# Kernel optimization log

Hardware: AMD Instinct MI355X
Metric: run time of the kernel (lower is better)

Reference implementation:

```python
import jax, jax.numpy as jnp
import numpy as np

N = 102400      # total nodes
B = 1024        # graphs in batch
NPG = 100       # nodes per graph
EPG = 1600      # edges per graph (avg degree 16)
E = B * EPG
D = 512
L = 3
EPS = 1e-5
SLOPE = 0.1     # LeakyReLU negative slope


def setup_inputs() -> dict:
    key = jax.random.key(0)
    k = jax.random.split(key, 6)
    node_feats = jax.random.normal(k[0], (N, D), dtype=jnp.float32)
    # within-graph random edges
    base = jnp.repeat(jnp.arange(B, dtype=jnp.int32) * NPG, EPG)  # [E]
    src = base + jax.random.randint(k[1], (E,), 0, NPG)
    dst = base + jax.random.randint(k[2], (E,), 0, NPG)
    graph_ids = jnp.repeat(jnp.arange(B, dtype=jnp.int32), NPG)   # [N]
    W = jax.random.normal(k[3], (L, D, D), dtype=jnp.float32) * 0.02
    gamma = jnp.ones((L, D), dtype=jnp.float32)
    beta = jnp.zeros((L, D), dtype=jnp.float32)
    lambdas = jnp.ones((L, 3), dtype=jnp.float32)
    return {"node_feats": node_feats, "src": src, "dst": dst,
            "graph_ids": graph_ids, "W": W, "gamma": gamma,
            "beta": beta, "lambdas": lambdas}


def _leaky(x):
    return jnp.where(x > 0, x, SLOPE * x)


def _united_norm(x, graph_ids, gamma, beta, lam):
    # combination of batch / graph / node standardizations, weighted by
    # learnable lambdas, then a shared affine (UnitedNormCommon).
    # batch norm over all nodes (training statistics, biased var)
    mu_b = x.mean(0)
    var_b = x.var(0)
    bn = (x - mu_b) * jax.lax.rsqrt(var_b + EPS)
    # graph norm: stats per graph segment
    mu_g = jax.ops.segment_sum(x, graph_ids, num_segments=B) / NPG
    ex2 = jax.ops.segment_sum(x * x, graph_ids, num_segments=B) / NPG
    var_g = ex2 - mu_g * mu_g
    gn = (x - mu_g[graph_ids]) * jax.lax.rsqrt(var_g + EPS)[graph_ids]
    # node norm: stats per node over feature dim
    mu_n = x.mean(-1, keepdims=True)
    var_n = x.var(-1, keepdims=True)
    nn_ = (x - mu_n) * jax.lax.rsqrt(var_n + EPS)
    mix = lam[0] * bn + lam[1] * gn + lam[2] * nn_
    return gamma * mix + beta


def reference(node_feats, src, dst, graph_ids, W, gamma, beta, lambdas):
    ones_e = jnp.ones((E,), dtype=node_feats.dtype)
    deg_out = jnp.clip(jax.ops.segment_sum(ones_e, src, num_segments=N), 1.0)
    deg_in = jnp.clip(jax.ops.segment_sum(ones_e, dst, num_segments=N), 1.0)
    c_out = jax.lax.rsqrt(deg_out)[:, None]  # D_out^{-1/2}
    c_in = jax.lax.rsqrt(deg_in)[:, None]    # D_in^{-1/2}

    h = node_feats
    embeddings = []
    for l in range(L):
        # GraphConv norm='both', bias=False: D_in^{-1/2} A D_out^{-1/2} h W
        msg = jax.ops.segment_sum((h * c_out)[src], dst, num_segments=N)
        h = (msg * c_in) @ W[l]
        h = _united_norm(h, graph_ids, gamma[l], beta[l], lambdas[l])
        h = _leaky(h)            # dropout=0 -> identity
        # dgl.mean_nodes readout per graph
        embeddings.append(jax.ops.segment_sum(h, graph_ids, num_segments=B) / NPG)
    out = jnp.concatenate(embeddings, axis=-1)   # JumpingKnowledge 'cat' -> [B, 3*D]
    return _leaky(out)
```

## Files before the change

### kernel.cpp

```cpp
#include <hip/hip_runtime.h>
#include <math.h>

#define NN 102400
#define BG 1024
#define NPG 100
#define EPG 1600
#define EE (BG*EPG)
#define DD 512
#define EPSN 1e-5f
#define SLOPE 0.1f

typedef short bf16x8 __attribute__((ext_vector_type(8)));
typedef float f32x4 __attribute__((ext_vector_type(4)));
typedef __attribute__((address_space(1))) const unsigned int gu32;
typedef __attribute__((address_space(3))) unsigned int lu32;

__device__ __forceinline__ void split_bf16(float v, unsigned short& hi, unsigned short& lo) {
    unsigned u = __float_as_uint(v);
    unsigned r = (u + 0x7FFFu + ((u >> 16) & 1u)) >> 16;
    hi = (unsigned short)r;
    float l = v - __uint_as_float(r << 16);
    unsigned ul = __float_as_uint(l);
    unsigned rl = (ul + 0x7FFFu + ((ul >> 16) & 1u)) >> 16;
    lo = (unsigned short)rl;
}


__global__ __launch_bounds__(256) void k_degrees(const int* __restrict__ src,
                                                 const int* __restrict__ dst,
                                                 float* degOut, float* degIn) {
    int e = blockIdx.x * 256 + threadIdx.x;
    atomicAdd(&degOut[src[e]], 1.0f);
    atomicAdd(&degIn[dst[e]], 1.0f);
}

__global__ __launch_bounds__(256) void k_deg_to_c(float* cOut, float* cIn) {
    int i = blockIdx.x * 256 + threadIdx.x;
    float a = cOut[i]; a = a < 1.0f ? 1.0f : a;
    cOut[i] = 1.0f / sqrtf(a);
    float b = cIn[i]; b = b < 1.0f ? 1.0f : b;
    cIn[i] = 1.0f / sqrtf(b);
}

__global__ __launch_bounds__(256) void k_build_A(const int* __restrict__ src,
                                                 const int* __restrict__ dst,
                                                 float* __restrict__ A) {
    int e = blockIdx.x * 256 + threadIdx.x;
    int s = src[e], d = dst[e];
    int g = s / NPG;
    int u = s - g * NPG;
    int v = d - g * NPG;
    atomicAdd(&A[(size_t)g * (NPG*NPG) + v * NPG + u], 1.0f);
}

__global__ __launch_bounds__(256) void k_scale_A(float* __restrict__ A,
                                                 const float* __restrict__ cOut,
                                                 const float* __restrict__ cIn) {
    int idx = blockIdx.x * 256 + threadIdx.x;
    int g = idx / (NPG*NPG);
    int r = idx - g * (NPG*NPG);
    int v = r / NPG;
    int u = r - v * NPG;
    A[idx] *= cIn[g*NPG + v] * cOut[g*NPG + u];
}

__global__ __launch_bounds__(256) void k_prepW(const float* __restrict__ W,
        unsigned short* __restrict__ wHiT, unsigned short* __restrict__ wLoT) {
    __shared__ float tile[64][65];
    int b = blockIdx.x;
    int l = b >> 6;
    int r8 = b & 63;
    int ko = (r8 >> 3) * 64, no = (r8 & 7) * 64;
    const float* Wl = W + (size_t)l * DD * DD;
    int t = threadIdx.x;
    #pragma unroll
    for (int i = 0; i < 16; ++i) {
        int idx = i * 256 + t;
        int r = idx >> 6, c = idx & 63;
        tile[r][c] = Wl[(size_t)(ko + r) * DD + no + c];
    }
    __syncthreads();
    size_t obase = (size_t)l * DD * DD;
    #pragma unroll
    for (int i = 0; i < 16; ++i) {
        int idx = i * 256 + t;
        int r = idx >> 6, c = idx & 63;
        float v = tile[c][r];
        unsigned short hi, lo;
        split_bf16(v, hi, lo);
        wHiT[obase + (size_t)(no + r) * DD + ko + c] = hi;
        wLoT[obase + (size_t)(no + r) * DD + ko + c] = lo;
    }
}


#define GG_DC 32

__global__ __launch_bounds__(256) void k_graph_gemm(const float* __restrict__ A,
                                                    const float* __restrict__ h,
                                                    unsigned short* __restrict__ msgHi,
                                                    unsigned short* __restrict__ msgLo) {
    __shared__ float As[NPG][108];
    __shared__ float hs[NPG][GG_DC];
    int g = blockIdx.x, tid = threadIdx.x;
    const float* Ag = A + (size_t)g * (NPG*NPG);
    size_t hbase = (size_t)g * NPG * DD;

    for (int i = tid; i < NPG*NPG; i += 256) {
        int v = i / NPG;
        As[v][i - v*NPG] = Ag[i];
    }

    int tx = tid & 7;
    int ty = tid >> 3;
    int v0 = ty * 4;

    for (int d0 = 0; d0 < DD; d0 += GG_DC) {
        int i0 = tid, i1 = tid + 256, i2 = tid + 512, i3 = tid + 768;
        float4 t0, t1, t2, t3;
        t0 = *(const float4*)&h[hbase + (size_t)(i0 >> 3) * DD + d0 + (i0 & 7) * 4];
        t1 = *(const float4*)&h[hbase + (size_t)(i1 >> 3) * DD + d0 + (i1 & 7) * 4];
        t2 = *(const float4*)&h[hbase + (size_t)(i2 >> 3) * DD + d0 + (i2 & 7) * 4];
        if (tid < 32)
            t3 = *(const float4*)&h[hbase + (size_t)(i3 >> 3) * DD + d0 + (i3 & 7) * 4];
        __syncthreads();
        *(float4*)&hs[i0 >> 3][(i0 & 7) * 4] = t0;
        *(float4*)&hs[i1 >> 3][(i1 & 7) * 4] = t1;
        *(float4*)&hs[i2 >> 3][(i2 & 7) * 4] = t2;
        if (tid < 32) *(float4*)&hs[i3 >> 3][(i3 & 7) * 4] = t3;
        __syncthreads();

        if (v0 < NPG) {
            float4 acc0 = make_float4(0,0,0,0);
            float4 acc1 = acc0, acc2 = acc0, acc3 = acc0;
            for (int u0 = 0; u0 < NPG; u0 += 4) {
                float4 a0 = *(float4*)&As[v0+0][u0];
                float4 a1 = *(float4*)&As[v0+1][u0];
                float4 a2 = *(float4*)&As[v0+2][u0];
                float4 a3 = *(float4*)&As[v0+3][u0];
                float4 h0 = *(float4*)&hs[u0+0][tx*4];
                float4 h1 = *(float4*)&hs[u0+1][tx*4];
                float4 h2 = *(float4*)&hs[u0+2][tx*4];
                float4 h3 = *(float4*)&hs[u0+3][tx*4];
#define GACC(ACC, AV) \
    ACC.x = fmaf(AV.x, h0.x, fmaf(AV.y, h1.x, fmaf(AV.z, h2.x, fmaf(AV.w, h3.x, ACC.x)))); \
    ACC.y = fmaf(AV.x, h0.y, fmaf(AV.y, h1.y, fmaf(AV.z, h2.y, fmaf(AV.w, h3.y, ACC.y)))); \
    ACC.z = fmaf(AV.x, h0.z, fmaf(AV.y, h1.z, fmaf(AV.z, h2.z, fmaf(AV.w, h3.z, ACC.z)))); \
    ACC.w = fmaf(AV.x, h0.w, fmaf(AV.y, h1.w, fmaf(AV.z, h2.w, fmaf(AV.w, h3.w, ACC.w))));
                GACC(acc0, a0) GACC(acc1, a1) GACC(acc2, a2) GACC(acc3, a3)
#undef GACC
            }
#define STORE_HL(ACC, ROW) { \
            ushort4 h4, l4; \
            split_bf16(ACC.x, h4.x, l4.x); split_bf16(ACC.y, h4.y, l4.y); \
            split_bf16(ACC.z, h4.z, l4.z); split_bf16(ACC.w, h4.w, l4.w); \
            *(ushort4*)&msgHi[hbase + (size_t)(ROW)*DD + d0 + tx*4] = h4; \
            *(ushort4*)&msgLo[hbase + (size_t)(ROW)*DD + d0 + tx*4] = l4; }
            STORE_HL(acc0, v0+0) STORE_HL(acc1, v0+1)
            STORE_HL(acc2, v0+2) STORE_HL(acc3, v0+3)
#undef STORE_HL
        }
    }
}


__global__ __launch_bounds__(256) void k_mfma_gemm(
        const unsigned short* __restrict__ aHi, const unsigned short* __restrict__ aLo,
        const unsigned short* __restrict__ bHiT, const unsigned short* __restrict__ bLoT,
        float* __restrict__ C) {
    __shared__ unsigned short lds[8192];
    int bx = blockIdx.x;
    int m0 = (bx >> 2) << 7;
    int n0 = (bx & 3) << 7;
    int tid = threadIdx.x;
    int wid = tid >> 6, lane = tid & 63;
    int wr = wid >> 1, wc = wid & 1;
    int lr = lane & 15, lk = (lane >> 4) * 8;

    f32x4 zero = {0.f, 0.f, 0.f, 0.f};
    f32x4 acc[4][4];
    #pragma unroll
    for (int i = 0; i < 4; ++i)
        #pragma unroll
        for (int j = 0; j < 4; ++j) acc[i][j] = zero;

    int rA0 = tid >> 2,           kq0 = (tid & 3) * 8;
    int rA1 = (tid + 256) >> 2,   kq1 = (tid & 3) * 8;
    unsigned short* lA0 = lds + wid * 512;
    unsigned short* lA1 = lds + 2048 + wid * 512;
    unsigned short* lB0 = lds + 4096 + wid * 512;
    unsigned short* lB1 = lds + 6144 + wid * 512;

    for (int kt = 0; kt < 48; ++kt) {
        int part = kt >> 4;
        const unsigned short* pA = (part == 1) ? aLo : aHi;
        const unsigned short* pB = (part == 2) ? bLoT : bHiT;
        int kl = (kt & 15) << 5;
        __syncthreads();
        __builtin_amdgcn_global_load_lds((gu32*)(pA + (size_t)(m0 + rA0) * DD + kl + kq0),
                                         (lu32*)lA0, 16, 0, 0);
        __builtin_amdgcn_global_load_lds((gu32*)(pA + (size_t)(m0 + rA1) * DD + kl + kq1),
                                         (lu32*)lA1, 16, 0, 0);
        __builtin_amdgcn_global_load_lds((gu32*)(pB + (size_t)(n0 + rA0) * DD + kl + kq0),
                                         (lu32*)lB0, 16, 0, 0);
        __builtin_amdgcn_global_load_lds((gu32*)(pB + (size_t)(n0 + rA1) * DD + kl + kq1),
                                         (lu32*)lB1, 16, 0, 0);
        __syncthreads();

        bf16x8 af[4], bfr[4];
        #pragma unroll
        for (int i = 0; i < 4; ++i) {
            af[i]  = *(const bf16x8*)(lds + (wr*64 + i*16 + lr) * 32 + lk);
            bfr[i] = *(const bf16x8*)(lds + 4096 + (wc*64 + i*16 + lr) * 32 + lk);
        }
        #pragma unroll
        for (int mi = 0; mi < 4; ++mi)
            #pragma unroll
            for (int ni = 0; ni < 4; ++ni)
                acc[mi][ni] = __builtin_amdgcn_mfma_f32_16x16x32_bf16(
                                  af[mi], bfr[ni], acc[mi][ni], 0, 0, 0);
    }

    #pragma unroll
    for (int mi = 0; mi < 4; ++mi) {
        int row0 = wr*64 + mi*16 + (lane >> 4) * 4;
        #pragma unroll
        for (int j = 0; j < 4; ++j) {
            int row = m0 + row0 + j;
            int col = n0 + wc*64 + lr;
            #pragma unroll
            for (int ni = 0; ni < 4; ++ni)
                C[(size_t)row * DD + col + ni*16] = acc[mi][ni][j];
        }
    }
}


__global__ __launch_bounds__(256) void k_stats(const float* __restrict__ x,
        float* __restrict__ mug, float* __restrict__ rsg,
        float* __restrict__ sumb, float* __restrict__ sumq) {
    int g = blockIdx.x, tid = threadIdx.x;
    size_t base = (size_t)g * NPG * DD;
    float s0 = 0, q0 = 0, s1 = 0, q1 = 0;
    for (int v = 0; v < NPG; ++v) {
        float a = x[base + (size_t)v*DD + tid];
        float b = x[base + (size_t)v*DD + tid + 256];
        s0 += a; q0 = fmaf(a, a, q0);
        s1 += b; q1 = fmaf(b, b, q1);
    }
    const float inv = 1.0f / NPG;
    float m0 = s0 * inv, m1 = s1 * inv;
    mug[(size_t)g*DD + tid]       = m0;
    mug[(size_t)g*DD + tid + 256] = m1;
    rsg[(size_t)g*DD + tid]       = 1.0f / sqrtf(fmaf(-m0, m0, q0*inv) + EPSN);
    rsg[(size_t)g*DD + tid + 256] = 1.0f / sqrtf(fmaf(-m1, m1, q1*inv) + EPSN);
    atomicAdd(&sumb[tid],       s0);
    atomicAdd(&sumq[tid],       q0);
    atomicAdd(&sumb[tid + 256], s1);
    atomicAdd(&sumq[tid + 256], q1);
}


__global__ __launch_bounds__(256) void k_norm(float* __restrict__ x,
        const float* __restrict__ mug, const float* __restrict__ rsg,
        const float* __restrict__ sumb, const float* __restrict__ sumq,
        const float* __restrict__ gamma, const float* __restrict__ beta,
        const float* __restrict__ lam, float* __restrict__ out, int l) {
    __shared__ float emb[4][DD];
    int g = blockIdx.x, tid = threadIdx.x;
    int lane = tid & 63, wave = tid >> 6;
    int cb = lane * 8;
    float l0 = lam[0], l1 = lam[1], l2 = lam[2];
    const float invN = 1.0f / NN;

    float P[8], Q[8], R[8];
    #pragma unroll
    for (int j = 0; j < 8; ++j) {
        int c = cb + j;
        float gm = gamma[c], bt = beta[c];
        float mg = mug[(size_t)g*DD + c], rg = rsg[(size_t)g*DD + c];
        float mb = sumb[c] * invN;
        float rb = 1.0f / sqrtf(fmaf(-mb, mb, sumq[c]*invN) + EPSN);
        P[j] = gm * (l0*rb + l1*rg);
        Q[j] = bt - gm * (l0*mb*rb + l1*mg*rg);
        R[j] = gm * l2;
    }

    float av[8];
    #pragma unroll
    for (int j = 0; j < 8; ++j) av[j] = 0.f;

    size_t base = (size_t)g * NPG * DD;
    for (int v = wave; v < NPG; v += 4) {
        float* rp = x + base + (size_t)v*DD + cb;
        float4 r0 = *(float4*)rp;
        float4 r1 = *(float4*)(rp + 4);
        float vals[8] = {r0.x, r0.y, r0.z, r0.w, r1.x, r1.y, r1.z, r1.w};
        float s = 0, q = 0;
        #pragma unroll
        for (int j = 0; j < 8; ++j) { s += vals[j]; q = fmaf(vals[j], vals[j], q); }
        #pragma unroll
        for (int off = 1; off < 64; off <<= 1) {
            s += __shfl_xor(s, off, 64);
            q += __shfl_xor(q, off, 64);
        }
        float mn = s * (1.0f/DD);
        float rn = 1.0f / sqrtf(fmaf(-mn, mn, q*(1.0f/DD)) + EPSN);
        float o[8];
        #pragma unroll
        for (int j = 0; j < 8; ++j) {
            float xv = vals[j];
            float nn = (xv - mn) * rn;
            float y = fmaf(P[j], xv, fmaf(R[j], nn, Q[j]));
            y = y > 0.f ? y : SLOPE * y;
            o[j] = y;
            av[j] += y;
        }
        *(float4*)rp       = make_float4(o[0], o[1], o[2], o[3]);
        *(float4*)(rp + 4) = make_float4(o[4], o[5], o[6], o[7]);
    }
    #pragma unroll
    for (int j = 0; j < 8; ++j) emb[wave][cb + j] = av[j];
    __syncthreads();
    for (int c = tid; c < DD; c += 256) {
        float e = (emb[0][c] + emb[1][c] + emb[2][c] + emb[3][c]) * (1.0f/NPG);
        e = e > 0.f ? e : SLOPE * e;
        out[(size_t)g * (3*DD) + l*DD + c] = e;
    }
}


extern "C" void kernel_launch(void* const* d_in, const int* in_sizes, int n_in,
                              void* d_out, int out_size, void* d_ws, size_t ws_size,
                              hipStream_t stream) {
    const float* nodeF   = (const float*)d_in[0];
    const int*   src     = (const int*)d_in[1];
    const int*   dst     = (const int*)d_in[2];
    const float* W       = (const float*)d_in[4];
    const float* gamma   = (const float*)d_in[5];
    const float* beta    = (const float*)d_in[6];
    const float* lambdas = (const float*)d_in[7];
    float* out = (float*)d_out;

    float* ws   = (float*)d_ws;
    float* cOut = ws;
    float* cIn  = cOut + NN;
    float* Abuf = cIn + NN;
    float* bufH = Abuf + (size_t)BG*NPG*NPG;
    float* mug  = bufH + (size_t)NN*DD;
    float* rsg  = mug  + (size_t)BG*DD;
    float* sumb = rsg  + (size_t)BG*DD;
    float* sumq = sumb + DD;
    unsigned short* msgHi = (unsigned short*)(sumq + DD);
    unsigned short* msgLo = msgHi + (size_t)NN*DD;
    unsigned short* wHiT  = msgLo + (size_t)NN*DD;
    unsigned short* wLoT  = wHiT  + (size_t)3*DD*DD;

    hipMemsetAsync(cOut, 0, 2*(size_t)NN*sizeof(float), stream);
    hipMemsetAsync(Abuf, 0, (size_t)BG*NPG*NPG*sizeof(float), stream);
    k_degrees<<<EE/256, 256, 0, stream>>>(src, dst, cOut, cIn);
    k_deg_to_c<<<NN/256, 256, 0, stream>>>(cOut, cIn);
    k_build_A<<<EE/256, 256, 0, stream>>>(src, dst, Abuf);
    k_scale_A<<<(BG*NPG*NPG)/256, 256, 0, stream>>>(Abuf, cOut, cIn);
    k_prepW<<<192, 256, 0, stream>>>(W, wHiT, wLoT);

    const float* hcur = nodeF;
    for (int l = 0; l < 3; ++l) {
        k_graph_gemm<<<BG, 256, 0, stream>>>(Abuf, hcur, msgHi, msgLo);
        k_mfma_gemm<<<(NN/128)*(DD/128), 256, 0, stream>>>(
            msgHi, msgLo, wHiT + (size_t)l*DD*DD, wLoT + (size_t)l*DD*DD, bufH);
        hipMemsetAsync(sumb, 0, 2*DD*sizeof(float), stream);
        k_stats<<<BG, 256, 0, stream>>>(bufH, mug, rsg, sumb, sumq);
        k_norm<<<BG, 256, 0, stream>>>(bufH, mug, rsg, sumb, sumq,
                                       gamma + l*DD, beta + l*DD, lambdas + l*3, out, l);
        hcur = bufH;
    }
}
```

Before: 2.365 ms.

## Double-buffer LDS in MFMA GEMM with swizzled layout and block remap

The split-bf16 MFMA GEMM now uses two LDS buffers. It issues the global-to-LDS load for the next K-tile before computing the current one, replacing the two barriers per iteration with one. Each thread's load assignment is XOR-permuted so that the 16-byte fragment reads from LDS avoid bank conflicts. Block indices are remapped so that neighbouring physical blocks spread across M strips, and launch bounds request 4 blocks per CU. In exchange, LDS use per block doubles, which may limit occupancy.

Result: faster. 2.006 ms (-15.2%).

```diff
diff --git a/kernel.cpp b/kernel.cpp
--- a/kernel.cpp
+++ b/kernel.cpp
@@ -164,18 +164,19 @@
 }
 
 
-__global__ __launch_bounds__(256) void k_mfma_gemm(
+__global__ __launch_bounds__(256, 4) void k_mfma_gemm(
         const unsigned short* __restrict__ aHi, const unsigned short* __restrict__ aLo,
         const unsigned short* __restrict__ bHiT, const unsigned short* __restrict__ bLoT,
         float* __restrict__ C) {
-    __shared__ unsigned short lds[8192];
-    int bx = blockIdx.x;
+    __shared__ unsigned short lds[16384];
+    int bphys = blockIdx.x;
+    int bx = (bphys & 7) * 400 + (bphys >> 3);
     int m0 = (bx >> 2) << 7;
     int n0 = (bx & 3) << 7;
     int tid = threadIdx.x;
     int wid = tid >> 6, lane = tid & 63;
     int wr = wid >> 1, wc = wid & 1;
-    int lr = lane & 15, lk = (lane >> 4) * 8;
+    int lr = lane & 15;
 
     f32x4 zero = {0.f, 0.f, 0.f, 0.f};
     f32x4 acc[4][4];
@@ -184,34 +185,48 @@
         #pragma unroll
         for (int j = 0; j < 4; ++j) acc[i][j] = zero;
 
-    int rA0 = tid >> 2,           kq0 = (tid & 3) * 8;
-    int rA1 = (tid + 256) >> 2,   kq1 = (tid & 3) * 8;
-    unsigned short* lA0 = lds + wid * 512;
-    unsigned short* lA1 = lds + 2048 + wid * 512;
-    unsigned short* lB0 = lds + 4096 + wid * 512;
-    unsigned short* lB1 = lds + 6144 + wid * 512;
-
+    int s0 = tid,        sr0 = s0 >> 2;
+    int s1 = tid + 256,  sr1 = s1 >> 2;
+    int r0 = sr0 ^ ((sr0 >> 2) & 1);  int c0 = (s0 & 3) ^ (r0 & 3);
+    int r1 = sr1 ^ ((sr1 >> 2) & 1);  int c1 = (s1 & 3) ^ (r1 & 3);
+    size_t gA0 = (size_t)(m0 + r0) * DD + c0 * 8;
+    size_t gA1 = (size_t)(m0 + r1) * DD + c1 * 8;
+    size_t gB0 = (size_t)(n0 + r0) * DD + c0 * 8;
+    size_t gB1 = (size_t)(n0 + r1) * DD + c1 * 8;
+
+    int aoff[4], boff[4];
+    int cq = lane >> 4;
+    #pragma unroll
+    for (int i = 0; i < 4; ++i) {
+        int ra = wr*64 + i*16 + lr;
+        aoff[i] = (ra ^ ((ra >> 2) & 1)) * 32 + ((cq ^ (ra & 3)) * 8);
+        int rb = wc*64 + i*16 + lr;
+        boff[i] = 4096 + (rb ^ ((rb >> 2) & 1)) * 32 + ((cq ^ (rb & 3)) * 8);
+    }
+
+#define STAGE(q, kt_) { \
+    int part_ = (kt_) >> 4; \
+    const unsigned short* pA_ = (part_ == 1) ? aLo : aHi;     \
+    const unsigned short* pB_ = (part_ == 2) ? bLoT : bHiT;   \
+    int kl_ = ((kt_) & 15) << 5; \
+    unsigned short* base_ = lds + (q) * 8192; \
+    __builtin_amdgcn_global_load_lds((gu32*)(pA_ + gA0 + kl_), (lu32*)(base_ + wid*512),        16, 0, 0); \
+    __builtin_amdgcn_global_load_lds((gu32*)(pA_ + gA1 + kl_), (lu32*)(base_ + 2048 + wid*512), 16, 0, 0); \
+    __builtin_amdgcn_global_load_lds((gu32*)(pB_ + gB0 + kl_), (lu32*)(base_ + 4096 + wid*512), 16, 0, 0); \
+    __builtin_amdgcn_global_load_lds((gu32*)(pB_ + gB1 + kl_), (lu32*)(base_ + 6144 + wid*512), 16, 0, 0); \
+}
+
+    STAGE(0, 0);
+    __syncthreads();
+    int cur = 0;
     for (int kt = 0; kt < 48; ++kt) {
-        int part = kt >> 4;
-        const unsigned short* pA = (part == 1) ? aLo : aHi;
-        const unsigned short* pB = (part == 2) ? bLoT : bHiT;
-        int kl = (kt & 15) << 5;
-        __syncthreads();
-        __builtin_amdgcn_global_load_lds((gu32*)(pA + (size_t)(m0 + rA0) * DD + kl + kq0),
-                                         (lu32*)lA0, 16, 0, 0);
-        __builtin_amdgcn_global_load_lds((gu32*)(pA + (size_t)(m0 + rA1) * DD + kl + kq1),
-                                         (lu32*)lA1, 16, 0, 0);
-        __builtin_amdgcn_global_load_lds((gu32*)(pB + (size_t)(n0 + rA0) * DD + kl + kq0),
-                                         (lu32*)lB0, 16, 0, 0);
-        __builtin_amdgcn_global_load_lds((gu32*)(pB + (size_t)(n0 + rA1) * DD + kl + kq1),
-                                         (lu32*)lB1, 16, 0, 0);
-        __syncthreads();
-
+        if (kt < 47) STAGE(cur ^ 1, kt + 1);
+        const unsigned short* bufp = lds + cur * 8192;
         bf16x8 af[4], bfr[4];
         #pragma unroll
         for (int i = 0; i < 4; ++i) {
-            af[i]  = *(const bf16x8*)(lds + (wr*64 + i*16 + lr) * 32 + lk);
-            bfr[i] = *(const bf16x8*)(lds + 4096 + (wc*64 + i*16 + lr) * 32 + lk);
+            af[i]  = *(const bf16x8*)(bufp + aoff[i]);
+            bfr[i] = *(const bf16x8*)(bufp + boff[i]);
         }
         #pragma unroll
         for (int mi = 0; mi < 4; ++mi)
@@ -219,7 +234,10 @@
             for (int ni = 0; ni < 4; ++ni)
                 acc[mi][ni] = __builtin_amdgcn_mfma_f32_16x16x32_bf16(
                                   af[mi], bfr[ni], acc[mi][ni], 0, 0, 0);
-    }
+        __syncthreads();
+        cur ^= 1;
+    }
+#undef STAGE
 
     #pragma unroll
     for (int mi = 0; mi < 4; ++mi) {
```
